# Performance work log

Measured on AMD Instinct MI355X. Metric: run time of the kernel, lower is better.

## Reference

```python
import jax, jax.numpy as jnp
import numpy as np

NUM_HEADS = 16

def setup_inputs() -> dict:
    key = jax.random.key(0)
    k1, k2, k3 = jax.random.split(key, 3)
    B, N, D = 4, 2048, 1024
    init_attn_std = D ** (-0.5)
    x = jax.random.normal(k1, (B, N, D), dtype=jnp.float32)
    qkv_w = jax.random.normal(k2, (D, 3 * D), dtype=jnp.float32) * init_attn_std
    proj_w = jax.random.normal(k3, (D, D), dtype=jnp.float32) * init_attn_std
    proj_b = jnp.zeros((D,), dtype=jnp.float32)
    return {"x": x, "qkv_w": qkv_w, "proj_w": proj_w, "proj_b": proj_b}

def reference(x, qkv_w, proj_w, proj_b):
    B, N, D = x.shape
    H = NUM_HEADS
    hd = D // H
    scale = hd ** (-0.5)
    # QKV projection (no bias, qkv_bias=False)
    qkv = (x @ qkv_w).reshape(B, N, 3, H, hd)
    q, k, v = jnp.moveaxis(qkv, 2, 0)  # each [B, N, H, hd]
    # scaled dot-product attention with causal mask (matches flax nn.dot_product_attention)
    scores = jnp.einsum('bqhd,bkhd->bhqk', q * scale, k)  # [B, H, N, N]
    causal = jnp.tril(jnp.ones((N, N), dtype=bool))
    big_neg = jnp.finfo(scores.dtype).min
    scores = jnp.where(causal, scores, big_neg)
    attn = jax.nn.softmax(scores, axis=-1)
    out = jnp.einsum('bhqk,bkhd->bqhd', attn, v).reshape(B, N, D)
    # output projection (proj_bias=True)
    return out @ proj_w + proj_b
```

## Files before the change

kernel.cpp:

```cpp
#include <hip/hip_runtime.h>

typedef __attribute__((ext_vector_type(8))) short sh8;
typedef __attribute__((ext_vector_type(8))) __bf16 bf8v;
typedef __attribute__((ext_vector_type(4))) float f4v;
typedef __attribute__((ext_vector_type(16))) float f16v;
typedef __attribute__((ext_vector_type(4))) unsigned u4v;

__device__ __forceinline__ float fast_exp2(float x) { return __builtin_amdgcn_exp2f(x); }

__device__ __forceinline__ unsigned short f2bf(float f) {
  unsigned u = __builtin_bit_cast(unsigned, f);
  u += 0x7fffu + ((u >> 16) & 1u);
  return (unsigned short)(u >> 16);
}
__device__ __forceinline__ float bf2f(unsigned short h) {
  unsigned u = ((unsigned)h) << 16;
  return __builtin_bit_cast(float, u);
}

__device__ __forceinline__ void glds16(const unsigned short* g, unsigned short* l) {
  __builtin_amdgcn_global_load_lds((const __attribute__((address_space(1))) void*)g,
                                   (__attribute__((address_space(3))) void*)l, 16, 0, 0);
}

__global__ __launch_bounds__(256) void cast_kernel(const float* __restrict__ in,
                                                   unsigned short* __restrict__ out) {
  const int idx = (blockIdx.x * 256 + threadIdx.x) * 4;
  const float4 v = *(const float4*)(in + idx);
  ushort4 o;
  o.x = f2bf(v.x); o.y = f2bf(v.y); o.z = f2bf(v.z); o.w = f2bf(v.w);
  *(ushort4*)(out + idx) = o;
}

__global__ __launch_bounds__(256) void transpose_cast_kernel(const float* __restrict__ in,
                                                             unsigned short* __restrict__ out,
                                                             int R, int C) {
  __shared__ float tile[32][33];
  const int c0 = blockIdx.x * 32, r0 = blockIdx.y * 32;
  const int tx = threadIdx.x, ty = threadIdx.y;
#pragma unroll
  for (int i = 0; i < 4; ++i)
    tile[ty + 8 * i][tx] = in[(size_t)(r0 + ty + 8 * i) * C + c0 + tx];
  __syncthreads();
#pragma unroll
  for (int i = 0; i < 4; ++i)
    out[(size_t)(c0 + ty + 8 * i) * R + r0 + tx] = f2bf(tile[tx][ty + 8 * i]);
}

template <int MODE>
__global__ __launch_bounds__(256, 2) void gemm_bf16_kernel(
    const unsigned short* __restrict__ A,
    const unsigned short* __restrict__ Bt,
    int M, int N, int K,
    unsigned short* __restrict__ q_out, unsigned short* __restrict__ k_out,
    unsigned short* __restrict__ v_out,
    const float* __restrict__ bias, float* __restrict__ c_out) {
  __shared__ alignas(16) unsigned short As[4 * 128 * 32];
  __shared__ alignas(16) unsigned short Bs[4 * 128 * 32];
  const int tid = threadIdx.x;
  const int lane = tid & 63;
  const int wave = tid >> 6;
  const int wr = (wave >> 1) * 64;
  const int wc = (wave & 1) * 64;
  const int bm = blockIdx.x * 128;
  const int bn = blockIdx.y * 128;
  const int fr = lane & 15;
  const int kq = lane >> 4;

  f4v acc[4][4] = {};

  const int r16 = lane >> 2;
  const int srcsl = (lane & 3) ^ ((r16 >> 1) & 3);
  const int rb0 = wave * 32, rb1 = wave * 32 + 16;

#define GSTAGE(g)                                                                            \
  {                                                                                          \
    const int _b = ((g) & 3) * 4096;                                                         \
    const int _k0 = (g) * 32;                                                                \
    glds16(&A[(size_t)(bm + rb0 + r16) * K + _k0 + srcsl * 8], &As[_b + rb0 * 32]);          \
    glds16(&A[(size_t)(bm + rb1 + r16) * K + _k0 + srcsl * 8], &As[_b + rb1 * 32]);          \
    glds16(&Bt[(size_t)(bn + rb0 + r16) * K + _k0 + srcsl * 8], &Bs[_b + rb0 * 32]);         \
    glds16(&Bt[(size_t)(bn + rb1 + r16) * K + _k0 + srcsl * 8], &Bs[_b + rb1 * 32]);         \
  }

  const int nT = K >> 5;
  GSTAGE(0);
  GSTAGE(1);

  const int rsl = (kq ^ ((fr >> 1) & 3)) * 8;

  for (int j = 0; j < nT; ++j) {
    const int buf = (j & 3) * 4096;
    if (j + 2 < nT) {
      GSTAGE(j + 2);
      asm volatile("s_waitcnt vmcnt(8)" ::: "memory");
    } else if (j + 1 < nT) {
      asm volatile("s_waitcnt vmcnt(4)" ::: "memory");
    } else {
      asm volatile("s_waitcnt vmcnt(0)" ::: "memory");
    }
    __builtin_amdgcn_s_barrier();

    bf8v af[4], bfv[4];
#pragma unroll
    for (int m = 0; m < 4; ++m)
      af[m] = __builtin_bit_cast(bf8v, *(const sh8*)&As[buf + (wr + m * 16 + fr) * 32 + rsl]);
#pragma unroll
    for (int n = 0; n < 4; ++n)
      bfv[n] = __builtin_bit_cast(bf8v, *(const sh8*)&Bs[buf + (wc + n * 16 + fr) * 32 + rsl]);
    __builtin_amdgcn_s_setprio(1);
#pragma unroll
    for (int m = 0; m < 4; ++m)
#pragma unroll
      for (int n = 0; n < 4; ++n)
        acc[m][n] = __builtin_amdgcn_mfma_f32_16x16x32_bf16(af[m], bfv[n], acc[m][n], 0, 0, 0);
    __builtin_amdgcn_s_setprio(0);
  }
#undef GSTAGE

  if (MODE == 0 && blockIdx.y >= 16) {
    unsigned short* Vlds = As;
    __builtin_amdgcn_s_barrier();
#pragma unroll
    for (int m = 0; m < 4; ++m)
#pragma unroll
      for (int n = 0; n < 4; ++n)
#pragma unroll
        for (int i = 0; i < 4; ++i) {
          const int rp = wr + m * 16 + kq * 4 + i;
          const int cp = wc + n * 16 + fr;
          Vlds[cp * 128 + (((rp >> 3) ^ (cp & 7)) << 3) + (rp & 7)] = f2bf(acc[m][n][i]);
        }
    __builtin_amdgcn_s_barrier();
    const int cp = tid >> 1, half = tid & 1;
    const int b = bm >> 11;
    const int h = ((bn - 2048) >> 6) + (cp >> 6);
    const int d = cp & 63;
    unsigned short* dst =
        v_out + ((size_t)((b * 16 + h) * 64 + d)) * 2048 + (bm & 2047) + half * 64;
#pragma unroll
    for (int s = 0; s < 8; ++s) {
      const int slot = (half * 8 + s) ^ (cp & 7);
      *(sh8*)(dst + s * 8) = *(const sh8*)&Vlds[cp * 128 + slot * 8];
    }
    return;
  }

#pragma unroll
  for (int m = 0; m < 4; ++m) {
#pragma unroll
    for (int n = 0; n < 4; ++n) {
#pragma unroll
      for (int i = 0; i < 4; ++i) {
        const int r = bm + wr + m * 16 + kq * 4 + i;
        const int c = bn + wc + n * 16 + fr;
        const float val = acc[m][n][i];
        if (MODE == 0) {
          const int b = r >> 11, nidx = r & 2047;
          const int rem = c & 1023;
          const int h = rem >> 6, d = rem & 63;
          const size_t off = ((size_t)((b * 16 + h) * 2048 + nidx)) * 64 + d;
          if (blockIdx.y < 8) q_out[off] = f2bf(val * 0.18033688f);
          else                k_out[off] = f2bf(val);
        } else {
          c_out[(size_t)r * N + c] = val + bias[c];
        }
      }
    }
  }
}

__global__ __launch_bounds__(256, 2) void attn_kernel(
    const unsigned short* __restrict__ Q, const unsigned short* __restrict__ Kg,
    const unsigned short* __restrict__ Vtg, unsigned short* __restrict__ O) {
  __shared__ alignas(16) unsigned short Ks[4][64 * 64];
  __shared__ alignas(16) unsigned short Vts[4][64 * 64];
  const int tid = threadIdx.x;
  const int lane = tid & 63;
  const int w = tid >> 6;
  const int q31 = lane & 31, hi = lane >> 5;
  const int sw = (lane & 7) << 3;
  const int wg = (blockIdx.x & 7) * 64 + (blockIdx.x >> 3);
  const int bh = wg >> 3;
  const int pair = wg & 7;
  const int qtA = pair, qtB = 15 - pair;
  const unsigned short* Qb = Q + (size_t)bh * (2048 * 64);
  const unsigned short* Kb = Kg + (size_t)bh * (2048 * 64);
  const unsigned short* Vtb = Vtg + (size_t)bh * (64 * 2048);
  const int q0wA = qtA * 128 + w * 32;
  const int q0wB = qtB * 128 + w * 32;

  bf8v qfA[4], qfB[4];
#pragma unroll
  for (int dk = 0; dk < 4; ++dk) {
    qfA[dk] = __builtin_bit_cast(bf8v, *(const sh8*)&Qb[(size_t)(q0wA + q31) * 64 + 8 * hi + 16 * dk]);
    qfB[dk] = __builtin_bit_cast(bf8v, *(const sh8*)&Qb[(size_t)(q0wB + q31) * 64 + 8 * hi + 16 * dk]);
  }

  f16v oA0 = {}, oA1 = {}, oB0 = {}, oB1 = {};
  float mA = -1e30f, lA = 0.f, mB = -1e30f, lB = 0.f;

  const int r8 = lane >> 3;
  const int gslot = (lane & 7) ^ r8;
  const int rb0 = w * 16, rb1 = w * 16 + 8;

#define STAGE(g)                                                                              \
  {                                                                                           \
    const int _b = (g) & 3;                                                                   \
    glds16(&Kb[(size_t)((g) * 64 + rb0 + r8) * 64 + gslot * 8], &Ks[_b][rb0 * 64]);           \
    glds16(&Kb[(size_t)((g) * 64 + rb1 + r8) * 64 + gslot * 8], &Ks[_b][rb1 * 64]);           \
    glds16(&Vtb[(size_t)(rb0 + r8) * 2048 + (g) * 64 + gslot * 8], &Vts[_b][rb0 * 64]);       \
    glds16(&Vtb[(size_t)(rb1 + r8) * 2048 + (g) * 64 + gslot * 8], &Vts[_b][rb1 * 64]);       \
  }

  auto body = [&](int j, int buf, int q0w, bf8v (&qf)[4], f16v& o0, f16v& o1,
                  float& m_i, float& l_i) {
    f16v s0 = {}, s1 = {};
    __builtin_amdgcn_s_setprio(1);
#pragma unroll
    for (int dk = 0; dk < 4; ++dk) {
      const int col = (8 * hi + 16 * dk) ^ sw;
      const bf8v k0 = __builtin_bit_cast(bf8v, *(const sh8*)&Ks[buf][q31 * 64 + col]);
      const bf8v k1 = __builtin_bit_cast(bf8v, *(const sh8*)&Ks[buf][(32 + q31) * 64 + col]);
      s0 = __builtin_amdgcn_mfma_f32_32x32x16_bf16(k0, qf[dk], s0, 0, 0, 0);
      s1 = __builtin_amdgcn_mfma_f32_32x32x16_bf16(k1, qf[dk], s1, 0, 0, 0);
    }
    __builtin_amdgcn_s_setprio(0);

    const int qg = q0w + q31;
    if (j * 64 + 63 > q0w) {
#pragma unroll
      for (int r = 0; r < 16; ++r) {
        const int kl = j * 64 + (r & 3) + 8 * (r >> 2) + 4 * hi;
        if (kl > qg) s0[r] = -1e30f;
        if (kl + 32 > qg) s1[r] = -1e30f;
      }
    }

    float mx = -1e30f;
#pragma unroll
    for (int r = 0; r < 16; ++r) mx = fmaxf(mx, fmaxf(s0[r], s1[r]));
    mx = fmaxf(mx, __shfl_xor(mx, 32));

    if (!__all(mx - m_i <= 8.f)) {
      const float mn = fmaxf(m_i, mx);
      const float alpha = fast_exp2(m_i - mn);
      m_i = mn;
      l_i *= alpha;
#pragma unroll
      for (int r = 0; r < 16; ++r) {
        const float ar = __shfl(alpha, (r & 3) + 8 * (r >> 2) + 4 * hi);
        o0[r] *= ar;
        o1[r] *= ar;
      }
    }

    float ps = 0.f;
#pragma unroll
    for (int r = 0; r < 16; ++r) {
      s0[r] = fast_exp2(s0[r] - m_i);
      s1[r] = fast_exp2(s1[r] - m_i);
      ps += s0[r] + s1[r];
    }
    ps += __shfl_xor(ps, 32);
    l_i += ps;

    unsigned w0[8], w1[8];
#pragma unroll
    for (int jj = 0; jj < 8; ++jj) {
      asm("v_cvt_pk_bf16_f32 %0, %1, %2" : "=v"(w0[jj]) : "v"(s0[2 * jj]), "v"(s0[2 * jj + 1]));
      asm("v_cvt_pk_bf16_f32 %0, %1, %2" : "=v"(w1[jj]) : "v"(s1[2 * jj]), "v"(s1[2 * jj + 1]));
    }

#pragma unroll
    for (int ks = 0; ks < 4; ++ks) {
      const int j0 = 4 * (ks & 1);
      unsigned x0 = (ks < 2 ? w0[j0 + 0] : w1[j0 + 0]);
      unsigned y0 = (ks < 2 ? w0[j0 + 2] : w1[j0 + 2]);
      unsigned x1 = (ks < 2 ? w0[j0 + 1] : w1[j0 + 1]);
      unsigned y1 = (ks < 2 ? w0[j0 + 3] : w1[j0 + 3]);
      asm("v_permlane32_swap_b32 %0, %1" : "+v"(x0), "+v"(y0));
      asm("v_permlane32_swap_b32 %0, %1" : "+v"(x1), "+v"(y1));
      u4v pw;
      pw[0] = x0; pw[1] = x1; pw[2] = y0; pw[3] = y1;
      const bf8v pa = __builtin_bit_cast(bf8v, pw);

      const int colv = (8 * hi + 16 * ks) ^ sw;
      const bf8v vf0 = __builtin_bit_cast(bf8v, *(const sh8*)&Vts[buf][q31 * 64 + colv]);
      const bf8v vf1 = __builtin_bit_cast(bf8v, *(const sh8*)&Vts[buf][(32 + q31) * 64 + colv]);
      __builtin_amdgcn_s_setprio(1);
      o0 = __builtin_amdgcn_mfma_f32_32x32x16_bf16(pa, vf0, o0, 0, 0, 0);
      o1 = __builtin_amdgcn_mfma_f32_32x32x16_bf16(pa, vf1, o1, 0, 0, 0);
      __builtin_amdgcn_s_setprio(0);
    }
  };

  const int b = bh >> 4, h = bh & 15;
  auto epi = [&](int q0w, f16v& o0, f16v& o1, float l_i) {
    const float rl = 1.f / l_i;
#pragma unroll
    for (int r = 0; r < 16; ++r) {
      const int cr = (r & 3) + 8 * (r >> 2) + 4 * hi;
      const float lr = __shfl(rl, cr);
      const size_t base = ((size_t)(b * 2048 + q0w + cr)) * 1024 + h * 64 + q31;
      O[base] = f2bf(o0[r] * lr);
      O[base + 32] = f2bf(o1[r] * lr);
    }
  };

  const int nA = 2 * qtA + 2;
  const int nT = 2 * qtB + 2;

  STAGE(0);
  STAGE(1);

  for (int j = 0; j < nT; ++j) {
    const int buf = j & 3;
    if (j + 2 < nT) {
      STAGE(j + 2);
      asm volatile("s_waitcnt vmcnt(8)" ::: "memory");
    } else if (j + 1 < nT) {
      asm volatile("s_waitcnt vmcnt(4)" ::: "memory");
    } else {
      asm volatile("s_waitcnt vmcnt(0)" ::: "memory");
    }
    __builtin_amdgcn_s_barrier();

    if (j < nA) body(j, buf, q0wA, qfA, oA0, oA1, mA, lA);
    body(j, buf, q0wB, qfB, oB0, oB1, mB, lB);

    if (j == nA - 1) epi(q0wA, oA0, oA1, lA);
  }
#undef STAGE

  epi(q0wB, oB0, oB1, lB);
}

extern "C" void kernel_launch(void* const* d_in, const int* in_sizes, int n_in,
                              void* d_out, int out_size, void* d_ws, size_t ws_size,
                              hipStream_t stream) {
  const float* x      = (const float*)d_in[0];
  const float* qkv_w  = (const float*)d_in[1];
  const float* proj_w = (const float*)d_in[2];
  const float* proj_b = (const float*)d_in[3];
  float* out = (float*)d_out;

  unsigned short* ws = (unsigned short*)d_ws;
  const size_t NE = (size_t)8192 * 1024;
  unsigned short* xb     = ws;
  unsigned short* wqkvT  = xb + NE;
  unsigned short* wprojT = wqkvT + (size_t)3072 * 1024;
  unsigned short* qb     = wprojT + (size_t)1024 * 1024;
  unsigned short* kb     = qb + NE;
  unsigned short* vt     = kb + NE;
  unsigned short* ab     = xb;

  cast_kernel<<<8192, 256, 0, stream>>>(x, xb);
  transpose_cast_kernel<<<dim3(96, 32), dim3(32, 8), 0, stream>>>(qkv_w, wqkvT, 1024, 3072);
  transpose_cast_kernel<<<dim3(32, 32), dim3(32, 8), 0, stream>>>(proj_w, wprojT, 1024, 1024);

  gemm_bf16_kernel<0><<<dim3(64, 24), 256, 0, stream>>>(
      xb, wqkvT, 8192, 3072, 1024, qb, kb, vt, nullptr, nullptr);

  attn_kernel<<<512, 256, 0, stream>>>(qb, kb, vt, ab);

  gemm_bf16_kernel<1><<<dim3(64, 8), 256, 0, stream>>>(
      ab, wprojT, 8192, 1024, 1024, nullptr, nullptr, nullptr, proj_b, out);
}
```

Baseline: 173.6 us.

## Replace 4-stage GEMM LDS pipeline with single-buffer synchronous loads for higher occupancy

Removes the 4-deep global_load_lds prefetch ring in the bf16 GEMM and loads each K-tile into a single buffer between two __syncthreads. LDS per block shrinks from 64KB to 32KB, and launch bounds rise to 4 blocks per CU, so more waves are resident to hide latency. In exchange, each block now stalls on memory every K step with no software overlap.

```diff
diff --git a/kernel.cpp b/kernel.cpp
--- a/kernel.cpp
+++ b/kernel.cpp
@@ -48,15 +48,16 @@
 }
 
 template <int MODE>
-__global__ __launch_bounds__(256, 2) void gemm_bf16_kernel(
+__global__ __launch_bounds__(256, 4) void gemm_bf16_kernel(
     const unsigned short* __restrict__ A,
     const unsigned short* __restrict__ Bt,
     int M, int N, int K,
     unsigned short* __restrict__ q_out, unsigned short* __restrict__ k_out,
     unsigned short* __restrict__ v_out,
     const float* __restrict__ bias, float* __restrict__ c_out) {
-  __shared__ alignas(16) unsigned short As[4 * 128 * 32];
-  __shared__ alignas(16) unsigned short Bs[4 * 128 * 32];
+  __shared__ alignas(16) unsigned short smem[128 * 128];
+  unsigned short* As = smem;
+  unsigned short* Bs = smem + 4096;
   const int tid = threadIdx.x;
   const int lane = tid & 63;
   const int wave = tid >> 6;
@@ -73,41 +74,25 @@
   const int srcsl = (lane & 3) ^ ((r16 >> 1) & 3);
   const int rb0 = wave * 32, rb1 = wave * 32 + 16;
 
-#define GSTAGE(g)                                                                            \
-  {                                                                                          \
-    const int _b = ((g) & 3) * 4096;                                                         \
-    const int _k0 = (g) * 32;                                                                \
-    glds16(&A[(size_t)(bm + rb0 + r16) * K + _k0 + srcsl * 8], &As[_b + rb0 * 32]);          \
-    glds16(&A[(size_t)(bm + rb1 + r16) * K + _k0 + srcsl * 8], &As[_b + rb1 * 32]);          \
-    glds16(&Bt[(size_t)(bn + rb0 + r16) * K + _k0 + srcsl * 8], &Bs[_b + rb0 * 32]);         \
-    glds16(&Bt[(size_t)(bn + rb1 + r16) * K + _k0 + srcsl * 8], &Bs[_b + rb1 * 32]);         \
-  }
-
+  const int rsl = (kq ^ ((fr >> 1) & 3)) * 8;
   const int nT = K >> 5;
-  GSTAGE(0);
-  GSTAGE(1);
-
-  const int rsl = (kq ^ ((fr >> 1) & 3)) * 8;
 
   for (int j = 0; j < nT; ++j) {
-    const int buf = (j & 3) * 4096;
-    if (j + 2 < nT) {
-      GSTAGE(j + 2);
-      asm volatile("s_waitcnt vmcnt(8)" ::: "memory");
-    } else if (j + 1 < nT) {
-      asm volatile("s_waitcnt vmcnt(4)" ::: "memory");
-    } else {
-      asm volatile("s_waitcnt vmcnt(0)" ::: "memory");
-    }
-    __builtin_amdgcn_s_barrier();
+    const int k0 = j * 32;
+    __syncthreads();
+    glds16(&A[(size_t)(bm + rb0 + r16) * K + k0 + srcsl * 8], &As[rb0 * 32]);
+    glds16(&A[(size_t)(bm + rb1 + r16) * K + k0 + srcsl * 8], &As[rb1 * 32]);
+    glds16(&Bt[(size_t)(bn + rb0 + r16) * K + k0 + srcsl * 8], &Bs[rb0 * 32]);
+    glds16(&Bt[(size_t)(bn + rb1 + r16) * K + k0 + srcsl * 8], &Bs[rb1 * 32]);
+    __syncthreads();
 
     bf8v af[4], bfv[4];
 #pragma unroll
     for (int m = 0; m < 4; ++m)
-      af[m] = __builtin_bit_cast(bf8v, *(const sh8*)&As[buf + (wr + m * 16 + fr) * 32 + rsl]);
+      af[m] = __builtin_bit_cast(bf8v, *(const sh8*)&As[(wr + m * 16 + fr) * 32 + rsl]);
 #pragma unroll
     for (int n = 0; n < 4; ++n)
-      bfv[n] = __builtin_bit_cast(bf8v, *(const sh8*)&Bs[buf + (wc + n * 16 + fr) * 32 + rsl]);
+      bfv[n] = __builtin_bit_cast(bf8v, *(const sh8*)&Bs[(wc + n * 16 + fr) * 32 + rsl]);
     __builtin_amdgcn_s_setprio(1);
 #pragma unroll
     for (int m = 0; m < 4; ++m)
@@ -116,11 +101,10 @@
         acc[m][n] = __builtin_amdgcn_mfma_f32_16x16x32_bf16(af[m], bfv[n], acc[m][n], 0, 0, 0);
     __builtin_amdgcn_s_setprio(0);
   }
-#undef GSTAGE
 
   if (MODE == 0 && blockIdx.y >= 16) {
-    unsigned short* Vlds = As;
-    __builtin_amdgcn_s_barrier();
+    unsigned short* Vlds = smem;
+    __syncthreads();
 #pragma unroll
     for (int m = 0; m < 4; ++m)
 #pragma unroll
@@ -131,7 +115,7 @@
           const int cp = wc + n * 16 + fr;
           Vlds[cp * 128 + (((rp >> 3) ^ (cp & 7)) << 3) + (rp & 7)] = f2bf(acc[m][n][i]);
         }
-    __builtin_amdgcn_s_barrier();
+    __syncthreads();
     const int cp = tid >> 1, half = tid & 1;
     const int b = bm >> 11;
     const int h = ((bn - 2048) >> 6) + (cp >> 6);
```

Measured after the change: 174.1 us. About the same (+0.3%).
